# Kernel tuning notes

Measured on AMD Instinct MI355X. Metric: run time of the kernel, lower is better.

The kernel has to match this reference:

```python
import jax, jax.numpy as jnp
import numpy as np

NUM_HEADS = 32
NUM_KV_HEADS = 8
HEAD_DIM = 64


def rotate_half(x):
    x1, x2 = jnp.split(x, 2, axis=-1)
    return jnp.concatenate((-x2, x1), axis=-1)


def setup_inputs() -> dict:
    key = jax.random.key(0)
    ks = jax.random.split(key, 7)
    B, S, H = 2, 2048, 2048
    hidden_states = jax.random.normal(ks[0], (B, S, H), dtype=jnp.float32)
    # RoPE angles: build realistic cos/sin from inv_freq for positions 0..S-1
    inv_freq = 1.0 / (10000.0 ** (np.arange(0, HEAD_DIM, 2, dtype=np.float32) / HEAD_DIM))
    t = np.arange(S, dtype=np.float32)
    freqs = np.outer(t, inv_freq)  # [S, HEAD_DIM/2]
    emb = np.concatenate([freqs, freqs], axis=-1)  # [S, HEAD_DIM]
    cos = jnp.broadcast_to(jnp.cos(emb)[None], (B, S, HEAD_DIM)).astype(jnp.float32)
    sin = jnp.broadcast_to(jnp.sin(emb)[None], (B, S, HEAD_DIM)).astype(jnp.float32)
    scale = 1.0 / np.sqrt(H)
    Wq = jax.random.normal(ks[1], (NUM_HEADS * HEAD_DIM, H), dtype=jnp.float32) * scale
    Wk = jax.random.normal(ks[2], (NUM_KV_HEADS * HEAD_DIM, H), dtype=jnp.float32) * scale
    Wv = jax.random.normal(ks[3], (NUM_KV_HEADS * HEAD_DIM, H), dtype=jnp.float32) * scale
    Wo = jax.random.normal(ks[4], (H, H), dtype=jnp.float32) * scale
    return {"hidden_states": hidden_states, "cos": cos, "sin": sin,
            "Wq": Wq, "Wk": Wk, "Wv": Wv, "Wo": Wo}


def reference(hidden_states, cos, sin, Wq, Wk, Wv, Wo):
    B, S, H = hidden_states.shape
    hd = HEAD_DIM
    # QKV projections (torch Linear: y = x @ W.T)
    q = jnp.einsum('bsi,oi->bso', hidden_states, Wq).reshape(B, S, NUM_HEADS, hd).transpose(0, 2, 1, 3)
    k = jnp.einsum('bsi,oi->bso', hidden_states, Wk).reshape(B, S, NUM_KV_HEADS, hd).transpose(0, 2, 1, 3)
    v = jnp.einsum('bsi,oi->bso', hidden_states, Wv).reshape(B, S, NUM_KV_HEADS, hd).transpose(0, 2, 1, 3)
    # RoPE: cos/sin [B,S,hd] -> [B,1,S,hd] broadcast over heads
    c = cos[:, None, :, :]
    s = sin[:, None, :, :]
    q = q * c + rotate_half(q) * s
    k = k * c + rotate_half(k) * s
    # GQA: repeat kv heads to match query heads
    groups = NUM_HEADS // NUM_KV_HEADS
    k = jnp.repeat(k, groups, axis=1)
    v = jnp.repeat(v, groups, axis=1)
    scaling = hd ** -0.5
    scores = jnp.einsum('bhqd,bhkd->bhqk', q, k) * scaling
    causal = jnp.tril(jnp.ones((S, S), dtype=bool))
    scores = jnp.where(causal, scores, jnp.finfo(scores.dtype).min)
    attn = jax.nn.softmax(scores, axis=-1)
    y = jnp.einsum('bhqk,bhkd->bhqd', attn, v)
    y = y.transpose(0, 2, 1, 3).reshape(B, S, H)
    return jnp.einsum('bsi,oi->bso', y, Wo)
```

## Files before the change

### kernel.cpp

```cpp
#include <hip/hip_runtime.h>

typedef __bf16 bf16_t;
typedef bf16_t bf16x8 __attribute__((ext_vector_type(8)));
typedef bf16_t bf16x4 __attribute__((ext_vector_type(4)));
typedef float f32x4 __attribute__((ext_vector_type(4)));
typedef float f32x16 __attribute__((ext_vector_type(16)));

#define MFMA16(a, b, c) __builtin_amdgcn_mfma_f32_16x16x32_bf16(a, b, c, 0, 0, 0)
#define MFMA32(a, b, c) __builtin_amdgcn_mfma_f32_32x32x16_bf16(a, b, c, 0, 0, 0)

#define GLOAD16(gsrc, ldst)                                            \
  __builtin_amdgcn_global_load_lds(                                    \
      (const __attribute__((address_space(1))) void*)(gsrc),           \
      (__attribute__((address_space(3))) void*)(ldst), 16, 0, 0)

constexpr int B_ = 2, S_ = 2048, H_ = 2048, NH = 32, NKV = 8, HD = 64;
constexpr int NQKV = NH * HD + 2 * NKV * HD;
constexpr int M_ROWS = B_ * S_;
constexpr float QSCALE = 0.125f * 1.4426950408889634f;

__global__ __launch_bounds__(256) void cvt_kernel(const float* __restrict__ in,
                                                  bf16_t* __restrict__ out, int n8) {
  int i = blockIdx.x * 256 + threadIdx.x;
  if (i >= n8) return;
  const float4* p = (const float4*)(in + (size_t)i * 8);
  float4 a = p[0], b = p[1];
  bf16x8 o;
  o[0] = (bf16_t)a.x; o[1] = (bf16_t)a.y; o[2] = (bf16_t)a.z; o[3] = (bf16_t)a.w;
  o[4] = (bf16_t)b.x; o[5] = (bf16_t)b.y; o[6] = (bf16_t)b.z; o[7] = (bf16_t)b.w;
  *(bf16x8*)(out + (size_t)i * 8) = o;
}

template <bool OUT_BF16>
__global__ __launch_bounds__(256) void gemm_bt(const bf16_t* __restrict__ A,
                                               const bf16_t* __restrict__ Bm,
                                               float* __restrict__ Cf,
                                               bf16_t* __restrict__ Cb,
                                               int M, int N, int K) {
  __shared__ __align__(16) bf16_t As[2][128 * 32];
  __shared__ __align__(16) bf16_t Bs[2][128 * 32];
  const int t = threadIdx.x;
  const int lane = t & 63, w = t >> 6;
  const int l15 = lane & 15, l4 = lane >> 4;
  const int wm = w >> 1, wn = w & 1;
  const long Ar0 = (long)blockIdx.y * 128;
  const long Br0 = (long)blockIdx.x * 128;
  const int nt = K >> 5;

  const int scol = ((lane & 3) ^ ((lane >> 3) & 3)) * 8;
  const int srow = lane >> 2;
  auto stage = [&](int kt, int buf) {
#pragma unroll
    for (int c = 0; c < 2; ++c) {
      const int i = w * 2 + c;
      const bf16_t* gA = A + (Ar0 + i * 16 + srow) * (long)K + kt * 32 + scol;
      const bf16_t* gB = Bm + (Br0 + i * 16 + srow) * (long)K + kt * 32 + scol;
      GLOAD16(gA, &As[buf][i * 512]);
      GLOAD16(gB, &Bs[buf][i * 512]);
    }
  };

  f32x4 acc[4][4] = {};
  stage(0, 0);
  __syncthreads();
  int cur = 0;
  const int rsw = l4 ^ ((l15 >> 1) & 3);
  for (int kt = 0; kt < nt; ++kt) {
    if (kt + 1 < nt) stage(kt + 1, cur ^ 1);
    bf16x8 af[4], bfr[4];
#pragma unroll
    for (int mf = 0; mf < 4; ++mf)
      af[mf] = *(const bf16x8*)&As[cur][(wm * 64 + mf * 16 + l15) * 32 + rsw * 8];
#pragma unroll
    for (int nf = 0; nf < 4; ++nf)
      bfr[nf] = *(const bf16x8*)&Bs[cur][(wn * 64 + nf * 16 + l15) * 32 + rsw * 8];
#pragma unroll
    for (int mf = 0; mf < 4; ++mf)
#pragma unroll
      for (int nf = 0; nf < 4; ++nf)
        acc[mf][nf] = MFMA16(af[mf], bfr[nf], acc[mf][nf]);
    __syncthreads();
    cur ^= 1;
  }
#pragma unroll
  for (int mf = 0; mf < 4; ++mf)
#pragma unroll
    for (int nf = 0; nf < 4; ++nf)
#pragma unroll
      for (int r = 0; r < 4; ++r) {
        long row = Ar0 + wm * 64 + mf * 16 + l4 * 4 + r;
        long col = Br0 + wn * 64 + nf * 16 + l15;
        float v = acc[mf][nf][r];
        if (OUT_BF16)
          Cb[row * N + col] = (bf16_t)v;
        else
          Cf[row * N + col] = v;
      }
}

__global__ __launch_bounds__(256) void rope_kernel(bf16_t* __restrict__ qkv,
                                                   const float* __restrict__ cosb,
                                                   const float* __restrict__ sinb) {
  long idx = (long)blockIdx.x * 256 + threadIdx.x;
  int d = (int)(idx & 31);
  long rest = idx >> 5;
  int head = (int)(rest % 40);
  long bs = rest / 40;
  long base = bs * NQKV + (head < 32 ? head * 64 : NH * HD + (head - 32) * 64);
  float c = cosb[bs * 64 + d];
  float sn = sinb[bs * 64 + d];
  float c2 = cosb[bs * 64 + d + 32];
  float s2 = sinb[bs * 64 + d + 32];
  float x1 = (float)qkv[base + d];
  float x2 = (float)qkv[base + d + 32];
  float y1 = x1 * c - x2 * sn;
  float y2 = x2 * c2 + x1 * s2;
  if (head < 32) { y1 *= QSCALE; y2 *= QSCALE; }
  qkv[base + d] = (bf16_t)y1;
  qkv[base + d + 32] = (bf16_t)y2;
}

__global__ __launch_bounds__(256) void v_transpose(const bf16_t* __restrict__ qkv,
                                                   bf16_t* __restrict__ vT) {
  long idx = (long)blockIdx.x * 256 + threadIdx.x;
  int s = (int)(idx & 2047);
  long rest = idx >> 11;
  int d = (int)(rest & 63);
  rest >>= 6;
  int kvh = (int)(rest & 7);
  int b = (int)(rest >> 3);
  vT[idx] = qkv[((long)(b * S_ + s)) * NQKV + NH * HD + NKV * HD + kvh * 64 + d];
}

__device__ __forceinline__ unsigned pkbf16(float lo, float hi) {
  union { bf16_t h[2]; unsigned u; } x;
  x.h[0] = (bf16_t)lo;
  x.h[1] = (bf16_t)hi;
  return x.u;
}

__global__ __launch_bounds__(256) void attn32_kernel(const bf16_t* __restrict__ qkv,
                                                     const bf16_t* __restrict__ vT,
                                                     bf16_t* __restrict__ y) {
  const int h = blockIdx.y;
  const int b = blockIdx.z;
  const int kvh = h >> 2;
  const int t = threadIdx.x, lane = t & 63, w = t >> 6;
  const int l31 = lane & 31, hd = lane >> 5;
  const long bS = (long)b * S_;

  __shared__ __align__(16) bf16_t Klds[2][64 * 64];
  __shared__ __align__(16) bf16_t Vlds[2][64 * 64];

  const bf16_t* kbase = qkv + bS * NQKV + NH * HD + kvh * 64;
  const bf16_t* vbase = vT + ((long)(b * NKV + kvh)) * 64 * S_;

  const int row0 = t >> 3;
  const int slot = t & 7;
  const int wslot8 = ((slot ^ (row0 & 7)) << 3);
  bf16x8 kreg0, kreg1, vreg0, vreg1;

  auto ldG = [&](int kv0) {
    const bf16_t* p = kbase + (long)(kv0 + row0) * NQKV + slot * 8;
    kreg0 = *(const bf16x8*)p;
    kreg1 = *(const bf16x8*)(p + 32L * NQKV);
    const bf16_t* pv = vbase + (long)row0 * S_ + kv0 + slot * 8;
    vreg0 = *(const bf16x8*)pv;
    vreg1 = *(const bf16x8*)(pv + 32L * S_);
  };
  auto wrLDS = [&](int buf) {
    *(bf16x8*)&Klds[buf][row0 * 64 + wslot8] = kreg0;
    *(bf16x8*)&Klds[buf][(row0 + 32) * 64 + wslot8] = kreg1;
    *(bf16x8*)&Vlds[buf][row0 * 64 + wslot8] = vreg0;
    *(bf16x8*)&Vlds[buf][(row0 + 32) * 64 + wslot8] = vreg1;
  };

  for (int half = 0; half < 2; ++half) {
    const int qt = half ? (int)blockIdx.x : 15 - (int)blockIdx.x;
    const int q0w = qt * 128 + w * 32;
    const int myq = q0w + l31;
    const int NT = qt * 2 + 2;

    const bf16_t* qp = qkv + (bS + myq) * NQKV + h * 64 + hd * 8;
    bf16x8 qf[4];
#pragma unroll
    for (int ks = 0; ks < 4; ++ks) qf[ks] = *(const bf16x8*)(qp + ks * 16);

    f32x16 yac[2] = {};
    float m = -1e30f, l = 0.f;

    ldG(0);
    wrLDS(0);
    __syncthreads();

    for (int kt = 0; kt < NT; ++kt) {
      const int buf = kt & 1;
      const int kv0 = kt * 64;
      if (kt + 1 < NT) ldG(kv0 + 64);

      if (kv0 <= q0w + 31) {
        f32x16 sac[2] = {};
#pragma unroll
        for (int ks = 0; ks < 4; ++ks)
#pragma unroll
          for (int kb = 0; kb < 2; ++kb) {
            const int row = kb * 32 + l31;
            const bf16x8 kf =
                *(const bf16x8*)&Klds[buf][row * 64 + (((2 * ks + hd) ^ (row & 7)) << 3)];
            sac[kb] = MFMA32(kf, qf[ks], sac[kb]);
          }
        if (kv0 + 63 > q0w) {
#pragma unroll
          for (int kb = 0; kb < 2; ++kb)
#pragma unroll
            for (int r = 0; r < 16; ++r) {
              const int kv = kv0 + kb * 32 + (r & 3) + 8 * (r >> 2) + 4 * hd;
              if (kv > myq) sac[kb][r] = -3.0e38f;
            }
        }
        float pm4[8], sm4[8];
#pragma unroll
        for (int g = 0; g < 8; ++g) {
          const int kb = g >> 2, r = (g & 3) * 4;
          pm4[g] = fmaxf(fmaxf(sac[kb][r], sac[kb][r + 1]),
                         fmaxf(sac[kb][r + 2], sac[kb][r + 3]));
        }
        float pm = fmaxf(fmaxf(fmaxf(pm4[0], pm4[1]), fmaxf(pm4[2], pm4[3])),
                         fmaxf(fmaxf(pm4[4], pm4[5]), fmaxf(pm4[6], pm4[7])));
        pm = fmaxf(pm, __shfl_xor(pm, 32, 64));
        if (!__all(pm <= m + 8.f)) {
          const float mnew = fmaxf(m, pm);
          const float sc = __builtin_amdgcn_exp2f(m - mnew);
          l *= sc;
          yac[0] *= sc;
          yac[1] *= sc;
          m = mnew;
        }
#pragma unroll
        for (int kb = 0; kb < 2; ++kb)
#pragma unroll
          for (int r = 0; r < 16; ++r)
            sac[kb][r] = __builtin_amdgcn_exp2f(sac[kb][r] - m);
#pragma unroll
        for (int g = 0; g < 8; ++g) {
          const int kb = g >> 2, r = (g & 3) * 4;
          sm4[g] = (sac[kb][r] + sac[kb][r + 1]) + (sac[kb][r + 2] + sac[kb][r + 3]);
        }
        float rs = ((sm4[0] + sm4[1]) + (sm4[2] + sm4[3])) +
                   ((sm4[4] + sm4[5]) + (sm4[6] + sm4[7]));
        rs += __shfl_xor(rs, 32, 64);
        l += rs;
#pragma unroll
        for (int ks = 0; ks < 4; ++ks) {
          const int kb = ks >> 1;
          const int Bv = 8 * (ks & 1);
          const unsigned p0 = pkbf16(sac[kb][Bv + 0], sac[kb][Bv + 1]);
          const unsigned p1 = pkbf16(sac[kb][Bv + 2], sac[kb][Bv + 3]);
          const unsigned p2 = pkbf16(sac[kb][Bv + 4], sac[kb][Bv + 5]);
          const unsigned p3 = pkbf16(sac[kb][Bv + 6], sac[kb][Bv + 7]);
          const unsigned xf0 = hd ? p0 : p2, xf1 = hd ? p1 : p3;
          const unsigned rc0 = __shfl_xor(xf0, 32, 64);
          const unsigned rc1 = __shfl_xor(xf1, 32, 64);
          union { unsigned u[4]; bf16x8 v; } pu;
          pu.u[0] = hd ? rc0 : p0;
          pu.u[1] = hd ? rc1 : p1;
          pu.u[2] = hd ? p2 : rc0;
          pu.u[3] = hd ? p3 : rc1;
#pragma unroll
          for (int db = 0; db < 2; ++db) {
            const int row = db * 32 + l31;
            const bf16x8 vf =
                *(const bf16x8*)&Vlds[buf][row * 64 + (((2 * ks + hd) ^ (row & 7)) << 3)];
            yac[db] = MFMA32(vf, pu.v, yac[db]);
          }
        }
      }

      if (kt + 1 < NT) wrLDS(buf ^ 1);
      __syncthreads();
    }

    const float inv = __builtin_amdgcn_rcpf(l);
    bf16_t* yp = y + (bS + myq) * (long)H_ + h * 64;
#pragma unroll
    for (int db = 0; db < 2; ++db)
#pragma unroll
      for (int g = 0; g < 4; ++g) {
        bf16x4 o;
        o[0] = (bf16_t)(yac[db][4 * g + 0] * inv);
        o[1] = (bf16_t)(yac[db][4 * g + 1] * inv);
        o[2] = (bf16_t)(yac[db][4 * g + 2] * inv);
        o[3] = (bf16_t)(yac[db][4 * g + 3] * inv);
        *(bf16x4*)(yp + db * 32 + 8 * g + 4 * hd) = o;
      }
  }
}

extern "C" void kernel_launch(void* const* d_in, const int* in_sizes, int n_in,
                              void* d_out, int out_size, void* d_ws, size_t ws_size,
                              hipStream_t stream) {
  const float* hs = (const float*)d_in[0];
  const float* cosb = (const float*)d_in[1];
  const float* sinb = (const float*)d_in[2];
  const float* Wq = (const float*)d_in[3];
  const float* Wk = (const float*)d_in[4];
  const float* Wv = (const float*)d_in[5];
  const float* Wo = (const float*)d_in[6];
  float* out = (float*)d_out;

  char* ws = (char*)d_ws;
  bf16_t* hsb  = (bf16_t*)(ws);
  bf16_t* wqkv = (bf16_t*)(ws + 16777216);
  bf16_t* wo   = (bf16_t*)(ws + 29360128);
  bf16_t* qkv  = (bf16_t*)(ws + 37748736);
  bf16_t* vT   = (bf16_t*)(ws + 62914560);
  bf16_t* yb   = (bf16_t*)(ws + 67108864);

  cvt_kernel<<<4096, 256, 0, stream>>>(hs, hsb, 1048576);
  cvt_kernel<<<2048, 256, 0, stream>>>(Wq, wqkv, 524288);
  cvt_kernel<<<512, 256, 0, stream>>>(Wk, wqkv + 2048 * 2048, 131072);
  cvt_kernel<<<512, 256, 0, stream>>>(Wv, wqkv + 2560 * 2048, 131072);
  cvt_kernel<<<2048, 256, 0, stream>>>(Wo, wo, 524288);

  gemm_bt<true><<<dim3(24, 32), 256, 0, stream>>>(hsb, wqkv, nullptr, qkv,
                                                  M_ROWS, NQKV, H_);
  rope_kernel<<<20480, 256, 0, stream>>>(qkv, cosb, sinb);
  v_transpose<<<8192, 256, 0, stream>>>(qkv, vT);
  attn32_kernel<<<dim3(8, 32, 2), 256, 0, stream>>>(qkv, vT, yb);
  gemm_bt<false><<<dim3(16, 32), 256, 0, stream>>>(yb, wo, out, nullptr,
                                                   M_ROWS, H_, H_);
}
```

Before: 231.6 us.

## Fuse RoPE and V transpose into QKV GEMM epilogue, shrink attention blocks

Moves the RoPE rotation, Q scaling and V transposition into the QKV GEMM epilogue, which removes two standalone elementwise kernels and their round trips through global memory. The three weight conversions are merged into one launch. The attention kernel now uses 128-thread blocks over 64-row query tiles, giving more blocks and finer causal balancing. It also swaps the shuffle-based P exchange for v_permlane32_swap, adds s_setprio around the MFMAs, and defers the cross-half row-sum reduction to the end. The epilogue now does scattered cos/sin loads and narrow transposed stores, and smaller blocks mean less K/V reuse per LDS tile.

```diff
diff --git a/kernel.cpp b/kernel.cpp
--- a/kernel.cpp
+++ b/kernel.cpp
@@ -31,11 +31,32 @@
   *(bf16x8*)(out + (size_t)i * 8) = o;
 }
 
-template <bool OUT_BF16>
+__global__ __launch_bounds__(256) void cvt3_kernel(const float* __restrict__ s0,
+                                                   const float* __restrict__ s1,
+                                                   const float* __restrict__ s2,
+                                                   bf16_t* __restrict__ out) {
+  int i = blockIdx.x * 256 + threadIdx.x;
+  const float* src;
+  long off;
+  if (i < 524288) { src = s0; off = i; }
+  else if (i < 655360) { src = s1; off = i - 524288; }
+  else { src = s2; off = i - 655360; }
+  const float4* p = (const float4*)(src + off * 8);
+  float4 a = p[0], b = p[1];
+  bf16x8 o;
+  o[0] = (bf16_t)a.x; o[1] = (bf16_t)a.y; o[2] = (bf16_t)a.z; o[3] = (bf16_t)a.w;
+  o[4] = (bf16_t)b.x; o[5] = (bf16_t)b.y; o[6] = (bf16_t)b.z; o[7] = (bf16_t)b.w;
+  *(bf16x8*)(out + (size_t)i * 8) = o;
+}
+
+template <int MODE>
 __global__ __launch_bounds__(256) void gemm_bt(const bf16_t* __restrict__ A,
                                                const bf16_t* __restrict__ Bm,
                                                float* __restrict__ Cf,
                                                bf16_t* __restrict__ Cb,
+                                               bf16_t* __restrict__ vTo,
+                                               const float* __restrict__ cosb,
+                                               const float* __restrict__ sinb,
                                                int M, int N, int K) {
   __shared__ __align__(16) bf16_t As[2][128 * 32];
   __shared__ __align__(16) bf16_t Bs[2][128 * 32];
@@ -82,54 +103,55 @@
     __syncthreads();
     cur ^= 1;
   }
-#pragma unroll
-  for (int mf = 0; mf < 4; ++mf)
-#pragma unroll
-    for (int nf = 0; nf < 4; ++nf)
-#pragma unroll
-      for (int r = 0; r < 4; ++r) {
-        long row = Ar0 + wm * 64 + mf * 16 + l4 * 4 + r;
-        long col = Br0 + wn * 64 + nf * 16 + l15;
-        float v = acc[mf][nf][r];
-        if (OUT_BF16)
-          Cb[row * N + col] = (bf16_t)v;
-        else
-          Cf[row * N + col] = v;
-      }
-}
-
-__global__ __launch_bounds__(256) void rope_kernel(bf16_t* __restrict__ qkv,
-                                                   const float* __restrict__ cosb,
-                                                   const float* __restrict__ sinb) {
-  long idx = (long)blockIdx.x * 256 + threadIdx.x;
-  int d = (int)(idx & 31);
-  long rest = idx >> 5;
-  int head = (int)(rest % 40);
-  long bs = rest / 40;
-  long base = bs * NQKV + (head < 32 ? head * 64 : NH * HD + (head - 32) * 64);
-  float c = cosb[bs * 64 + d];
-  float sn = sinb[bs * 64 + d];
-  float c2 = cosb[bs * 64 + d + 32];
-  float s2 = sinb[bs * 64 + d + 32];
-  float x1 = (float)qkv[base + d];
-  float x2 = (float)qkv[base + d + 32];
-  float y1 = x1 * c - x2 * sn;
-  float y2 = x2 * c2 + x1 * s2;
-  if (head < 32) { y1 *= QSCALE; y2 *= QSCALE; }
-  qkv[base + d] = (bf16_t)y1;
-  qkv[base + d + 32] = (bf16_t)y2;
-}
-
-__global__ __launch_bounds__(256) void v_transpose(const bf16_t* __restrict__ qkv,
-                                                   bf16_t* __restrict__ vT) {
-  long idx = (long)blockIdx.x * 256 + threadIdx.x;
-  int s = (int)(idx & 2047);
-  long rest = idx >> 11;
-  int d = (int)(rest & 63);
-  rest >>= 6;
-  int kvh = (int)(rest & 7);
-  int b = (int)(rest >> 3);
-  vT[idx] = qkv[((long)(b * S_ + s)) * NQKV + NH * HD + NKV * HD + kvh * 64 + d];
+
+  if (MODE == 0) {
+#pragma unroll
+    for (int mf = 0; mf < 4; ++mf)
+#pragma unroll
+      for (int nf = 0; nf < 4; ++nf)
+#pragma unroll
+        for (int r = 0; r < 4; ++r) {
+          long row = Ar0 + wm * 64 + mf * 16 + l4 * 4 + r;
+          long col = Br0 + wn * 64 + nf * 16 + l15;
+          Cf[row * N + col] = acc[mf][nf][r];
+        }
+  } else {
+    const long col0 = Br0 + wn * 64;
+    if (col0 < 2560) {
+      const float scl = (col0 < 2048) ? QSCALE : 1.0f;
+#pragma unroll
+      for (int mf = 0; mf < 4; ++mf) {
+        const long row = Ar0 + wm * 64 + mf * 16 + l4 * 4;
+#pragma unroll
+        for (int nf = 0; nf < 2; ++nf) {
+          const int d = nf * 16 + l15;
+#pragma unroll
+          for (int r = 0; r < 4; ++r) {
+            const float c = cosb[(row + r) * 64 + d] * scl;
+            const float s = sinb[(row + r) * 64 + d] * scl;
+            const float x1 = acc[mf][nf][r], x2 = acc[mf][nf + 2][r];
+            Cb[(row + r) * N + col0 + d]      = (bf16_t)(x1 * c - x2 * s);
+            Cb[(row + r) * N + col0 + d + 32] = (bf16_t)(x2 * c + x1 * s);
+          }
+        }
+      }
+    } else {
+#pragma unroll
+      for (int mf = 0; mf < 4; ++mf) {
+        const long row = Ar0 + wm * 64 + mf * 16 + l4 * 4;
+        const int bb = (int)(row >> 11);
+        const int ss = (int)(row & 2047);
+#pragma unroll
+        for (int nf = 0; nf < 4; ++nf) {
+          const int vd = (int)(col0 - 2560) + nf * 16 + l15;
+          bf16x4 o;
+#pragma unroll
+          for (int r = 0; r < 4; ++r) o[r] = (bf16_t)acc[mf][nf][r];
+          *(bf16x4*)&vTo[((long)bb * 512 + vd) * 2048 + ss] = o;
+        }
+      }
+    }
+  }
 }
 
 __device__ __forceinline__ unsigned pkbf16(float lo, float hi) {
@@ -139,7 +161,7 @@
   return x.u;
 }
 
-__global__ __launch_bounds__(256) void attn32_kernel(const bf16_t* __restrict__ qkv,
+__global__ __launch_bounds__(128) void attn32_kernel(const bf16_t* __restrict__ qkv,
                                                      const bf16_t* __restrict__ vT,
                                                      bf16_t* __restrict__ y) {
   const int h = blockIdx.y;
@@ -158,28 +180,28 @@
   const int row0 = t >> 3;
   const int slot = t & 7;
   const int wslot8 = ((slot ^ (row0 & 7)) << 3);
-  bf16x8 kreg0, kreg1, vreg0, vreg1;
+  bf16x8 kreg[4], vreg[4];
 
   auto ldG = [&](int kv0) {
-    const bf16_t* p = kbase + (long)(kv0 + row0) * NQKV + slot * 8;
-    kreg0 = *(const bf16x8*)p;
-    kreg1 = *(const bf16x8*)(p + 32L * NQKV);
-    const bf16_t* pv = vbase + (long)row0 * S_ + kv0 + slot * 8;
-    vreg0 = *(const bf16x8*)pv;
-    vreg1 = *(const bf16x8*)(pv + 32L * S_);
+#pragma unroll
+    for (int c = 0; c < 4; ++c) {
+      kreg[c] = *(const bf16x8*)(kbase + (long)(kv0 + row0 + 16 * c) * NQKV + slot * 8);
+      vreg[c] = *(const bf16x8*)(vbase + (long)(row0 + 16 * c) * S_ + kv0 + slot * 8);
+    }
   };
   auto wrLDS = [&](int buf) {
-    *(bf16x8*)&Klds[buf][row0 * 64 + wslot8] = kreg0;
-    *(bf16x8*)&Klds[buf][(row0 + 32) * 64 + wslot8] = kreg1;
-    *(bf16x8*)&Vlds[buf][row0 * 64 + wslot8] = vreg0;
-    *(bf16x8*)&Vlds[buf][(row0 + 32) * 64 + wslot8] = vreg1;
+#pragma unroll
+    for (int c = 0; c < 4; ++c) {
+      *(bf16x8*)&Klds[buf][(row0 + 16 * c) * 64 + wslot8] = kreg[c];
+      *(bf16x8*)&Vlds[buf][(row0 + 16 * c) * 64 + wslot8] = vreg[c];
+    }
   };
 
   for (int half = 0; half < 2; ++half) {
-    const int qt = half ? (int)blockIdx.x : 15 - (int)blockIdx.x;
-    const int q0w = qt * 128 + w * 32;
+    const int qt = half ? (int)blockIdx.x : 31 - (int)blockIdx.x;
+    const int q0w = qt * 64 + w * 32;
     const int myq = q0w + l31;
-    const int NT = qt * 2 + 2;
+    const int NT = qt + 1;
 
     const bf16_t* qp = qkv + (bS + myq) * NQKV + h * 64 + hd * 8;
     bf16x8 qf[4];
@@ -198,88 +220,85 @@
       const int kv0 = kt * 64;
       if (kt + 1 < NT) ldG(kv0 + 64);
 
-      if (kv0 <= q0w + 31) {
-        f32x16 sac[2] = {};
-#pragma unroll
-        for (int ks = 0; ks < 4; ++ks)
-#pragma unroll
-          for (int kb = 0; kb < 2; ++kb) {
-            const int row = kb * 32 + l31;
-            const bf16x8 kf =
-                *(const bf16x8*)&Klds[buf][row * 64 + (((2 * ks + hd) ^ (row & 7)) << 3)];
-            sac[kb] = MFMA32(kf, qf[ks], sac[kb]);
+      f32x16 sac[2] = {};
+      __builtin_amdgcn_s_setprio(1);
+#pragma unroll
+      for (int ks = 0; ks < 4; ++ks)
+#pragma unroll
+        for (int kb = 0; kb < 2; ++kb) {
+          const int row = kb * 32 + l31;
+          const bf16x8 kf =
+              *(const bf16x8*)&Klds[buf][row * 64 + (((2 * ks + hd) ^ (row & 7)) << 3)];
+          sac[kb] = MFMA32(kf, qf[ks], sac[kb]);
+        }
+      __builtin_amdgcn_s_setprio(0);
+      if (kv0 + 63 > q0w) {
+#pragma unroll
+        for (int kb = 0; kb < 2; ++kb)
+#pragma unroll
+          for (int r = 0; r < 16; ++r) {
+            const int kv = kv0 + kb * 32 + (r & 3) + 8 * (r >> 2) + 4 * hd;
+            if (kv > myq) sac[kb][r] = -3.0e38f;
           }
-        if (kv0 + 63 > q0w) {
-#pragma unroll
-          for (int kb = 0; kb < 2; ++kb)
-#pragma unroll
-            for (int r = 0; r < 16; ++r) {
-              const int kv = kv0 + kb * 32 + (r & 3) + 8 * (r >> 2) + 4 * hd;
-              if (kv > myq) sac[kb][r] = -3.0e38f;
-            }
-        }
-        float pm4[8], sm4[8];
-#pragma unroll
-        for (int g = 0; g < 8; ++g) {
-          const int kb = g >> 2, r = (g & 3) * 4;
-          pm4[g] = fmaxf(fmaxf(sac[kb][r], sac[kb][r + 1]),
-                         fmaxf(sac[kb][r + 2], sac[kb][r + 3]));
-        }
-        float pm = fmaxf(fmaxf(fmaxf(pm4[0], pm4[1]), fmaxf(pm4[2], pm4[3])),
-                         fmaxf(fmaxf(pm4[4], pm4[5]), fmaxf(pm4[6], pm4[7])));
-        pm = fmaxf(pm, __shfl_xor(pm, 32, 64));
-        if (!__all(pm <= m + 8.f)) {
-          const float mnew = fmaxf(m, pm);
-          const float sc = __builtin_amdgcn_exp2f(m - mnew);
-          l *= sc;
-          yac[0] *= sc;
-          yac[1] *= sc;
-          m = mnew;
-        }
-#pragma unroll
-        for (int kb = 0; kb < 2; ++kb)
-#pragma unroll
-          for (int r = 0; r < 16; ++r)
-            sac[kb][r] = __builtin_amdgcn_exp2f(sac[kb][r] - m);
-#pragma unroll
-        for (int g = 0; g < 8; ++g) {
-          const int kb = g >> 2, r = (g & 3) * 4;
-          sm4[g] = (sac[kb][r] + sac[kb][r + 1]) + (sac[kb][r + 2] + sac[kb][r + 3]);
-        }
-        float rs = ((sm4[0] + sm4[1]) + (sm4[2] + sm4[3])) +
-                   ((sm4[4] + sm4[5]) + (sm4[6] + sm4[7]));
-        rs += __shfl_xor(rs, 32, 64);
-        l += rs;
-#pragma unroll
-        for (int ks = 0; ks < 4; ++ks) {
-          const int kb = ks >> 1;
-          const int Bv = 8 * (ks & 1);
-          const unsigned p0 = pkbf16(sac[kb][Bv + 0], sac[kb][Bv + 1]);
-          const unsigned p1 = pkbf16(sac[kb][Bv + 2], sac[kb][Bv + 3]);
-          const unsigned p2 = pkbf16(sac[kb][Bv + 4], sac[kb][Bv + 5]);
-          const unsigned p3 = pkbf16(sac[kb][Bv + 6], sac[kb][Bv + 7]);
-          const unsigned xf0 = hd ? p0 : p2, xf1 = hd ? p1 : p3;
-          const unsigned rc0 = __shfl_xor(xf0, 32, 64);
-          const unsigned rc1 = __shfl_xor(xf1, 32, 64);
-          union { unsigned u[4]; bf16x8 v; } pu;
-          pu.u[0] = hd ? rc0 : p0;
-          pu.u[1] = hd ? rc1 : p1;
-          pu.u[2] = hd ? p2 : rc0;
-          pu.u[3] = hd ? p3 : rc1;
-#pragma unroll
-          for (int db = 0; db < 2; ++db) {
-            const int row = db * 32 + l31;
-            const bf16x8 vf =
-                *(const bf16x8*)&Vlds[buf][row * 64 + (((2 * ks + hd) ^ (row & 7)) << 3)];
-            yac[db] = MFMA32(vf, pu.v, yac[db]);
-          }
-        }
+      }
+      float pm4[8], sm4[8];
+#pragma unroll
+      for (int g = 0; g < 8; ++g) {
+        const int kb = g >> 2, r = (g & 3) * 4;
+        pm4[g] = fmaxf(fmaxf(sac[kb][r], sac[kb][r + 1]),
+                       fmaxf(sac[kb][r + 2], sac[kb][r + 3]));
+      }
+      float pm = fmaxf(fmaxf(fmaxf(pm4[0], pm4[1]), fmaxf(pm4[2], pm4[3])),
+                       fmaxf(fmaxf(pm4[4], pm4[5]), fmaxf(pm4[6], pm4[7])));
+      pm = fmaxf(pm, __shfl_xor(pm, 32, 64));
+      if (!__all(pm <= m + 8.f)) {
+        const float mnew = fmaxf(m, pm);
+        const float sc = __builtin_amdgcn_exp2f(m - mnew);
+        l *= sc;
+        yac[0] *= sc;
+        yac[1] *= sc;
+        m = mnew;
+      }
+#pragma unroll
+      for (int kb = 0; kb < 2; ++kb)
+#pragma unroll
+        for (int r = 0; r < 16; ++r)
+          sac[kb][r] = __builtin_amdgcn_exp2f(sac[kb][r] - m);
+#pragma unroll
+      for (int g = 0; g < 8; ++g) {
+        const int kb = g >> 2, r = (g & 3) * 4;
+        sm4[g] = (sac[kb][r] + sac[kb][r + 1]) + (sac[kb][r + 2] + sac[kb][r + 3]);
+      }
+      l += ((sm4[0] + sm4[1]) + (sm4[2] + sm4[3])) +
+           ((sm4[4] + sm4[5]) + (sm4[6] + sm4[7]));
+#pragma unroll
+      for (int ks = 0; ks < 4; ++ks) {
+        const int kb = ks >> 1;
+        const int Bv = 8 * (ks & 1);
+        unsigned a0 = pkbf16(sac[kb][Bv + 0], sac[kb][Bv + 1]);
+        unsigned b0 = pkbf16(sac[kb][Bv + 4], sac[kb][Bv + 5]);
+        unsigned a1 = pkbf16(sac[kb][Bv + 2], sac[kb][Bv + 3]);
+        unsigned b1 = pkbf16(sac[kb][Bv + 6], sac[kb][Bv + 7]);
+        asm("v_permlane32_swap_b32 %0, %1" : "+v"(a0), "+v"(b0));
+        asm("v_permlane32_swap_b32 %0, %1" : "+v"(a1), "+v"(b1));
+        union { unsigned u[4]; bf16x8 v; } pu;
+        pu.u[0] = a0; pu.u[1] = a1; pu.u[2] = b0; pu.u[3] = b1;
+        __builtin_amdgcn_s_setprio(1);
+#pragma unroll
+        for (int db = 0; db < 2; ++db) {
+          const int row = db * 32 + l31;
+          const bf16x8 vf =
+              *(const bf16x8*)&Vlds[buf][row * 64 + (((2 * ks + hd) ^ (row & 7)) << 3)];
+          yac[db] = MFMA32(vf, pu.v, yac[db]);
+        }
+        __builtin_amdgcn_s_setprio(0);
       }
 
       if (kt + 1 < NT) wrLDS(buf ^ 1);
       __syncthreads();
     }
 
+    l += __shfl_xor(l, 32, 64);
     const float inv = __builtin_amdgcn_rcpf(l);
     bf16_t* yp = y + (bS + myq) * (long)H_ + h * 64;
 #pragma unroll
@@ -317,16 +336,12 @@
   bf16_t* yb   = (bf16_t*)(ws + 67108864);
 
   cvt_kernel<<<4096, 256, 0, stream>>>(hs, hsb, 1048576);
-  cvt_kernel<<<2048, 256, 0, stream>>>(Wq, wqkv, 524288);
-  cvt_kernel<<<512, 256, 0, stream>>>(Wk, wqkv + 2048 * 2048, 131072);
-  cvt_kernel<<<512, 256, 0, stream>>>(Wv, wqkv + 2560 * 2048, 131072);
+  cvt3_kernel<<<3072, 256, 0, stream>>>(Wq, Wk, Wv, wqkv);
   cvt_kernel<<<2048, 256, 0, stream>>>(Wo, wo, 524288);
 
-  gemm_bt<true><<<dim3(24, 32), 256, 0, stream>>>(hsb, wqkv, nullptr, qkv,
-                                                  M_ROWS, NQKV, H_);
-  rope_kernel<<<20480, 256, 0, stream>>>(qkv, cosb, sinb);
-  v_transpose<<<8192, 256, 0, stream>>>(qkv, vT);
-  attn32_kernel<<<dim3(8, 32, 2), 256, 0, stream>>>(qkv, vT, yb);
-  gemm_bt<false><<<dim3(16, 32), 256, 0, stream>>>(yb, wo, out, nullptr,
-                                                   M_ROWS, H_, H_);
-}
+  gemm_bt<1><<<dim3(24, 32), 256, 0, stream>>>(hsb, wqkv, nullptr, qkv, vT,
+                                               cosb, sinb, M_ROWS, NQKV, H_);
+  attn32_kernel<<<dim3(16, 32, 2), 128, 0, stream>>>(qkv, vT, yb);
+  gemm_bt<0><<<dim3(16, 32), 256, 0, stream>>>(yb, wo, out, nullptr, nullptr,
+                                               nullptr, nullptr, M_ROWS, H_, H_);
+}
```

New measurement: 236.7 us. 2.2% more time.
